# Kernel tuning notes

Measured on AMD Instinct MI355X. Metric: run time of the kernel, lower is better.

## Reference

```python
import jax, jax.numpy as jnp
import numpy as np

N_NODES = 100000
N_EDGES = 3200000
IN_F, HID_F, OUT_F = 512, 64, 16


def setup_inputs() -> dict:
    key = jax.random.key(0)
    k1, k2, k3, k4 = jax.random.split(key, 4)
    x = jax.random.normal(k1, (N_NODES, IN_F), dtype=jnp.float32)
    edge_index = jax.random.randint(k2, (2, N_EDGES), 0, N_NODES, dtype=jnp.int64)
    W1 = jax.random.normal(k3, (IN_F, HID_F), dtype=jnp.float32) * (1.0 / np.sqrt(IN_F))
    b1 = jnp.zeros((HID_F,), dtype=jnp.float32)
    W2 = jax.random.normal(k4, (HID_F, OUT_F), dtype=jnp.float32) * (1.0 / np.sqrt(HID_F))
    b2 = jnp.zeros((OUT_F,), dtype=jnp.float32)
    return {"x": x, "edge_index": edge_index, "W1": W1, "b1": b1, "W2": W2, "b2": b2}


def _gcn_norm(edge_index, n_nodes):
    # add self-loops (GCNConv default), edge_weight = 1
    loop = jnp.arange(n_nodes, dtype=edge_index.dtype)
    src = jnp.concatenate([edge_index[0], loop])
    dst = jnp.concatenate([edge_index[1], loop])
    ones = jnp.ones(src.shape[0], dtype=jnp.float32)
    deg = jax.ops.segment_sum(ones, dst, num_segments=n_nodes)
    dinv = jnp.where(deg > 0, jax.lax.rsqrt(deg), 0.0)
    norm = dinv[src] * dinv[dst]  # symmetric normalization D^-1/2 A D^-1/2
    return src, dst, norm


def _gcn_conv(h, src, dst, norm, W, b, n_nodes):
    h = h @ W                                 # project first (small GEMM)
    msg = h[src] * norm[:, None]              # gather + scale  [E+N, F_out]
    agg = jax.ops.segment_sum(msg, dst, num_segments=n_nodes)  # scatter-add
    return agg + b


def reference(x, edge_index, W1, b1, W2, b2):
    n = x.shape[0]
    src, dst, norm = _gcn_norm(edge_index, n)
    h = jax.nn.relu(_gcn_conv(x, src, dst, norm, W1, b1, n))
    # F.dropout with training=False is identity (eval-mode reference)
    h = _gcn_conv(h, src, dst, norm, W2, b2, n)
    return jax.nn.log_softmax(h, axis=1)
```

## Files before the change

### kernel.cpp

```cpp
#include <hip/hip_runtime.h>

#define NN    100000
#define NE    3200000
#define INF_  512
#define HIDF  64
#define OUTF  16
#define BR    128
#define NBUCK ((NN + BR - 1) / BR)
#define NGRP  8
#define SLICE 704
#define BSLOT (NGRP * SLICE)
#define NCUR  (NBUCK * NGRP)
#define NSLOT 72
#define EBLK  16384
#define NFB   ((NE + EBLK - 1) / EBLK)

typedef __bf16 bf16x8 __attribute__((ext_vector_type(8)));
typedef float  f32x4  __attribute__((ext_vector_type(4)));

__device__ inline unsigned short f2bfu(float f) {
    unsigned u = __builtin_bit_cast(unsigned, f);
    u += 0x7FFFu + ((u >> 16) & 1u);
    return (unsigned short)(u >> 16);
}
__device__ inline __bf16 bfbits(unsigned short h) {
    return __builtin_bit_cast(__bf16, h);
}
__device__ inline float bf2f(unsigned short h) {
    unsigned u = (unsigned)h << 16;
    return __builtin_bit_cast(float, u);
}

__global__ __launch_bounds__(256) void k_binit(int* __restrict__ bcur) {
    int i = blockIdx.x * 256 + threadIdx.x;
    if (i < NCUR) bcur[i] = (i >> 3) * BSLOT + (i & 7) * SLICE;
}

__global__ __launch_bounds__(256) void k_wconv(const float* __restrict__ W1,
                                               unsigned short* __restrict__ w1c) {
    int i = blockIdx.x * 256 + threadIdx.x;
    if (i < INF_ * HIDF) {
        int k = i >> 6, n = i & 63;
        w1c[((k >> 2) * 64 + n) * 4 + (k & 3)] = f2bfu(W1[i]);
    }
}

__global__ __launch_bounds__(256) void k_fillA(const int* __restrict__ src,
                                               const int* __restrict__ dst,
                                               int* __restrict__ bcur,
                                               unsigned int* __restrict__ pairs) {
    __shared__ int hist[NBUCK];
    __shared__ int rbase[NBUCK];
    int t = threadIdx.x;
    int e0 = blockIdx.x * EBLK;
    int e1 = (e0 + EBLK < NE) ? e0 + EBLK : NE;
    int grp = (int)(((long long)blockIdx.x * NGRP) / NFB);

    for (int b = t; b < NBUCK; b += 256) hist[b] = 0;
    __syncthreads();
    for (int e = e0 + t; e < e1; e += 256)
        atomicAdd(&hist[dst[e] >> 7], 1);
    __syncthreads();
    for (int b = t; b < NBUCK; b += 256) {
        int c = hist[b];
        rbase[b] = c ? atomicAdd(&bcur[b * NGRP + grp], c) : 0;
        hist[b] = 0;
    }
    __syncthreads();
    for (int e = e0 + t; e < e1; e += 256) {
        int s = src[e], d = dst[e];
        int b = d >> 7;
        int slot = atomicAdd(&hist[b], 1);
        pairs[rbase[b] + slot] = ((unsigned)s << 7) | (unsigned)(d & 127);
    }
}

__global__ __launch_bounds__(256) void k_fillB(const int* __restrict__ bcur,
                                               const unsigned int* __restrict__ pairs,
                                               int* __restrict__ re,
                                               float* __restrict__ dinv,
                                               int* __restrict__ csr) {
    __shared__ int cur_s[BR];
    int b  = blockIdx.x;
    int t  = threadIdx.x;
    int n0 = b * BR;
    int ncount = ((n0 + BR < NN) ? BR : NN - n0);

    if (t < BR) cur_s[t] = (n0 + t) * NSLOT;
    __syncthreads();

    for (int g = 0; g < NGRP; ++g) {
        int s0 = b * BSLOT + g * SLICE;
        int s1 = bcur[b * NGRP + g];
        for (int j = s0 + t; j < s1; j += 256) {
            unsigned int p = pairs[j];
            int pos = atomicAdd(&cur_s[p & 127u], 1);
            csr[pos] = (int)(p >> 7);
        }
    }
    __syncthreads();

    if (t < ncount) {
        int endp = cur_s[t];
        int n = n0 + t;
        re[n]   = endp;
        dinv[n] = rsqrtf((float)(endp - n * NSLOT + 1));
    }
}

#define GM 64

__global__ __launch_bounds__(256) void k_gemm1(const float* __restrict__ x,
                                               const unsigned short* __restrict__ w1c,
                                               const float* __restrict__ dinv,
                                               unsigned short* __restrict__ h1s) {
    __shared__ unsigned short bs[8192];
    int t    = threadIdx.x;
    int lane = t & 63;
    int w    = t >> 6;
    int m    = lane & 15;
    int kg   = lane >> 4;
    int mb   = blockIdx.x * GM;

    int rowi = mb + w * 16 + m;
    size_t xrow = (size_t)((rowi < NN) ? rowi : NN - 1);
    const float* xp = x + xrow * INF_ + kg * 4;

    f32x4 acc0 = {0.f,0.f,0.f,0.f}, acc1 = acc0, acc2 = acc0, acc3 = acc0;

    const uint4* w1c4 = (const uint4*)w1c;
    uint4* bs4 = (uint4*)bs;

    for (int kc = 0; kc < 4; ++kc) {
#pragma unroll
        for (int i = 0; i < 4; ++i)
            bs4[t + i * 256] = w1c4[kc * 1024 + t + i * 256];
        __syncthreads();

#pragma unroll
        for (int ks = 0; ks < 4; ++ks) {
            int ksg = kc * 4 + ks;
            float4 xa = *(const float4*)(xp + ksg * 32);
            float4 xb = *(const float4*)(xp + ksg * 32 + 16);
            bf16x8 A;
            A[0] = bfbits(f2bfu(xa.x)); A[1] = bfbits(f2bfu(xa.y));
            A[2] = bfbits(f2bfu(xa.z)); A[3] = bfbits(f2bfu(xa.w));
            A[4] = bfbits(f2bfu(xb.x)); A[5] = bfbits(f2bfu(xb.y));
            A[6] = bfbits(f2bfu(xb.z)); A[7] = bfbits(f2bfu(xb.w));

            int qq0 = ks * 8 + kg;
            int qq1 = qq0 + 4;
#pragma unroll
            for (int n0t = 0; n0t < 4; ++n0t) {
                ushort4 b0 = *(const ushort4*)&bs[(qq0 * 64 + n0t * 16 + m) * 4];
                ushort4 b1 = *(const ushort4*)&bs[(qq1 * 64 + n0t * 16 + m) * 4];
                bf16x8 B;
                B[0] = bfbits(b0.x); B[1] = bfbits(b0.y);
                B[2] = bfbits(b0.z); B[3] = bfbits(b0.w);
                B[4] = bfbits(b1.x); B[5] = bfbits(b1.y);
                B[6] = bfbits(b1.z); B[7] = bfbits(b1.w);
                f32x4 c = (n0t == 0) ? acc0 : (n0t == 1) ? acc1 : (n0t == 2) ? acc2 : acc3;
                c = __builtin_amdgcn_mfma_f32_16x16x32_bf16(A, B, c, 0, 0, 0);
                if      (n0t == 0) acc0 = c;
                else if (n0t == 1) acc1 = c;
                else if (n0t == 2) acc2 = c;
                else               acc3 = c;
            }
        }
        __syncthreads();
    }

#pragma unroll
    for (int r = 0; r < 4; ++r) {
        int node = mb + w * 16 + kg * 4 + r;
        if (node < NN) {
            float dv = dinv[node];
            size_t o = (size_t)node * HIDF + m;
            h1s[o +  0] = f2bfu(acc0[r] * dv);
            h1s[o + 16] = f2bfu(acc1[r] * dv);
            h1s[o + 32] = f2bfu(acc2[r] * dv);
            h1s[o + 48] = f2bfu(acc3[r] * dv);
        }
    }
}

__global__ __launch_bounds__(256) void k_hid2(const int* __restrict__ re,
                                              const int* __restrict__ csr,
                                              const float* __restrict__ dinv,
                                              const unsigned short* __restrict__ h1s,
                                              const float* __restrict__ b1,
                                              const float* __restrict__ W2,
                                              unsigned short* __restrict__ h2s) {
    __shared__ float w2s[HIDF * OUTF];
    __shared__ float b1s[HIDF];
    __shared__ float hbuf[4][HIDF];
    int t = threadIdx.x;
    for (int i = t; i < HIDF * OUTF; i += 256) w2s[i] = W2[i];
    if (t < HIDF) b1s[t] = b1[t];
    __syncthreads();

    int l = t & 63;
    int w = t >> 6;
    int g = l >> 4;
    int q = l & 15;
    int n = __builtin_amdgcn_readfirstlane(blockIdx.x * 4 + w);
    int row = n * NSLOT;
    int end = re[n];
    float dn = dinv[n];

    float a0 = 0.f, a1 = 0.f, a2 = 0.f, a3 = 0.f;

    int j = row;
    for (; j + 16 <= end; j += 16) {
        int4 scA = *(const int4*)&csr[j];
        int4 scB = *(const int4*)&csr[j + 4];
        int4 scC = *(const int4*)&csr[j + 8];
        int4 scD = *(const int4*)&csr[j + 12];
        int sA = (g & 2) ? ((g & 1) ? scA.w : scA.z) : ((g & 1) ? scA.y : scA.x);
        int sB = (g & 2) ? ((g & 1) ? scB.w : scB.z) : ((g & 1) ? scB.y : scB.x);
        int sC = (g & 2) ? ((g & 1) ? scC.w : scC.z) : ((g & 1) ? scC.y : scC.x);
        int sD = (g & 2) ? ((g & 1) ? scD.w : scD.z) : ((g & 1) ? scD.y : scD.x);
        ushort4 hA = *(const ushort4*)&h1s[(unsigned)(sA * HIDF + q * 4)];
        ushort4 hB = *(const ushort4*)&h1s[(unsigned)(sB * HIDF + q * 4)];
        ushort4 hC = *(const ushort4*)&h1s[(unsigned)(sC * HIDF + q * 4)];
        ushort4 hD = *(const ushort4*)&h1s[(unsigned)(sD * HIDF + q * 4)];
        a0 += (bf2f(hA.x) + bf2f(hB.x)) + (bf2f(hC.x) + bf2f(hD.x));
        a1 += (bf2f(hA.y) + bf2f(hB.y)) + (bf2f(hC.y) + bf2f(hD.y));
        a2 += (bf2f(hA.z) + bf2f(hB.z)) + (bf2f(hC.z) + bf2f(hD.z));
        a3 += (bf2f(hA.w) + bf2f(hB.w)) + (bf2f(hC.w) + bf2f(hD.w));
    }
    for (; j + 8 <= end; j += 8) {
        int4 scA = *(const int4*)&csr[j];
        int4 scB = *(const int4*)&csr[j + 4];
        int sA = (g & 2) ? ((g & 1) ? scA.w : scA.z) : ((g & 1) ? scA.y : scA.x);
        int sB = (g & 2) ? ((g & 1) ? scB.w : scB.z) : ((g & 1) ? scB.y : scB.x);
        ushort4 hA = *(const ushort4*)&h1s[(unsigned)(sA * HIDF + q * 4)];
        ushort4 hB = *(const ushort4*)&h1s[(unsigned)(sB * HIDF + q * 4)];
        a0 += bf2f(hA.x) + bf2f(hB.x);
        a1 += bf2f(hA.y) + bf2f(hB.y);
        a2 += bf2f(hA.z) + bf2f(hB.z);
        a3 += bf2f(hA.w) + bf2f(hB.w);
    }
    if (j + 4 <= end) {
        int4 sc = *(const int4*)&csr[j];
        int s = (g & 2) ? ((g & 1) ? sc.w : sc.z) : ((g & 1) ? sc.y : sc.x);
        ushort4 h = *(const ushort4*)&h1s[(unsigned)(s * HIDF + q * 4)];
        a0 += bf2f(h.x); a1 += bf2f(h.y); a2 += bf2f(h.z); a3 += bf2f(h.w);
        j += 4;
    }
    if (j + g < end) {
        int s = csr[j + g];
        ushort4 h = *(const ushort4*)&h1s[(unsigned)(s * HIDF + q * 4)];
        a0 += bf2f(h.x); a1 += bf2f(h.y); a2 += bf2f(h.z); a3 += bf2f(h.w);
    }

    a0 += __shfl_xor(a0, 16); a1 += __shfl_xor(a1, 16);
    a2 += __shfl_xor(a2, 16); a3 += __shfl_xor(a3, 16);
    a0 += __shfl_xor(a0, 32); a1 += __shfl_xor(a1, 32);
    a2 += __shfl_xor(a2, 32); a3 += __shfl_xor(a3, 32);

    ushort4 hs = *(const ushort4*)&h1s[(unsigned)(n * HIDF + q * 4)];
    a0 = fmaxf(fmaf(dn, a0 + bf2f(hs.x), b1s[q * 4 + 0]), 0.f);
    a1 = fmaxf(fmaf(dn, a1 + bf2f(hs.y), b1s[q * 4 + 1]), 0.f);
    a2 = fmaxf(fmaf(dn, a2 + bf2f(hs.z), b1s[q * 4 + 2]), 0.f);
    a3 = fmaxf(fmaf(dn, a3 + bf2f(hs.w), b1s[q * 4 + 3]), 0.f);
    if (g == 0) *(float4*)&hbuf[w][q * 4] = make_float4(a0, a1, a2, a3);
    __syncthreads();

    int o  = l & 15;
    int kg = l >> 4;
    const float* hb = hbuf[w];
    float s = 0.f;
#pragma unroll
    for (int i = 0; i < 16; ++i) {
        int k = kg * 16 + i;
        s = fmaf(hb[k], w2s[k * OUTF + o], s);
    }
    s += __shfl_xor(s, 16);
    s += __shfl_xor(s, 32);
    if (l < 16) h2s[(unsigned)(n * OUTF + o)] = f2bfu(dn * s);
}

__global__ __launch_bounds__(256) void k_out2(const int* __restrict__ re,
                                              const int* __restrict__ csr,
                                              const float* __restrict__ dinv,
                                              const unsigned short* __restrict__ h2s,
                                              const float* __restrict__ b2,
                                              float* __restrict__ out) {
    int t = blockIdx.x * 256 + threadIdx.x;
    int n = t >> 4;
    int f = t & 15;
    if (n >= NN) return;
    int row = n * NSLOT, end = re[n];
    float dn = dinv[n];
    float acc = bf2f(h2s[(unsigned)(n * OUTF + f)]);

    int j = row;
    for (; j + 8 <= end; j += 8) {
        int s0 = csr[j],     s1 = csr[j + 1], s2 = csr[j + 2], s3 = csr[j + 3];
        int s4 = csr[j + 4], s5 = csr[j + 5], s6 = csr[j + 6], s7 = csr[j + 7];
        float v0 = bf2f(h2s[(unsigned)(s0 * OUTF + f)]);
        float v1 = bf2f(h2s[(unsigned)(s1 * OUTF + f)]);
        float v2 = bf2f(h2s[(unsigned)(s2 * OUTF + f)]);
        float v3 = bf2f(h2s[(unsigned)(s3 * OUTF + f)]);
        float v4 = bf2f(h2s[(unsigned)(s4 * OUTF + f)]);
        float v5 = bf2f(h2s[(unsigned)(s5 * OUTF + f)]);
        float v6 = bf2f(h2s[(unsigned)(s6 * OUTF + f)]);
        float v7 = bf2f(h2s[(unsigned)(s7 * OUTF + f)]);
        acc += ((v0 + v1) + (v2 + v3)) + ((v4 + v5) + (v6 + v7));
    }
    for (; j + 4 <= end; j += 4) {
        int s0 = csr[j], s1 = csr[j + 1], s2 = csr[j + 2], s3 = csr[j + 3];
        float v0 = bf2f(h2s[(unsigned)(s0 * OUTF + f)]);
        float v1 = bf2f(h2s[(unsigned)(s1 * OUTF + f)]);
        float v2 = bf2f(h2s[(unsigned)(s2 * OUTF + f)]);
        float v3 = bf2f(h2s[(unsigned)(s3 * OUTF + f)]);
        acc += (v0 + v1) + (v2 + v3);
    }
    for (; j < end; ++j)
        acc += bf2f(h2s[(unsigned)(csr[j] * OUTF + f)]);

    float v = fmaf(dn, acc, b2[f]);

    float m = v;
#pragma unroll
    for (int mask = 1; mask < 16; mask <<= 1)
        m = fmaxf(m, __shfl_xor(m, mask, 16));
    float ex = __expf(v - m);
    float s  = ex;
#pragma unroll
    for (int mask = 1; mask < 16; mask <<= 1)
        s += __shfl_xor(s, mask, 16);
    out[(size_t)n * OUTF + f] = v - (m + __logf(s));
}

extern "C" void kernel_launch(void* const* d_in, const int* in_sizes, int n_in,
                              void* d_out, int out_size, void* d_ws, size_t ws_size,
                              hipStream_t stream) {
    const float* x  = (const float*)d_in[0];
    const int*   ei = (const int*)d_in[1];
    const float* W1 = (const float*)d_in[2];
    const float* b1 = (const float*)d_in[3];
    const float* W2 = (const float*)d_in[4];
    const float* b2 = (const float*)d_in[5];
    float*       out = (float*)d_out;

    char*  ws = (char*)d_ws;
    size_t o  = 0;
    auto alloc = [&](size_t bytes) {
        void* p = ws + o;
        o = (o + bytes + 1023) & ~(size_t)1023;
        return p;
    };
    int*            bcur  = (int*)           alloc((size_t)NCUR * 4);
    int*            re    = (int*)           alloc((size_t)NN * 4);
    int*            csr   = (int*)           alloc((size_t)NN * NSLOT * 4);
    unsigned int*   pairs = (unsigned int*)  alloc((size_t)NBUCK * BSLOT * 4);
    float*          dinv  = (float*)         alloc((size_t)NN * 4);
    unsigned short* w1c   = (unsigned short*)alloc((size_t)INF_ * HIDF * 2);
    unsigned short* h1s   = (unsigned short*)alloc((size_t)NN * HIDF * 2);
    unsigned short* h2s   = (unsigned short*)alloc((size_t)NN * OUTF * 2);
    if (o > ws_size) return;

    const int* esrc = ei;
    const int* edst = ei + NE;

    k_binit <<<(NCUR + 255) / 256, 256, 0, stream>>>(bcur);
    k_wconv <<<(INF_ * HIDF + 255) / 256, 256, 0, stream>>>(W1, w1c);
    k_fillA <<<NFB, 256, 0, stream>>>(esrc, edst, bcur, pairs);
    k_fillB <<<NBUCK, 256, 0, stream>>>(bcur, pairs, re, dinv, csr);

    k_gemm1 <<<(NN + GM - 1) / GM, 256, 0, stream>>>(x, w1c, dinv, h1s);
    k_hid2  <<<NN / 4, 256, 0, stream>>>(re, csr, dinv, h1s, b1, W2, h2s);
    k_out2  <<<(NN * OUTF + 255) / 256, 256, 0, stream>>>(re, csr, dinv, h2s, b2, out);
}
```

Baseline: 259.6 us.

## Overlap edge bucketing with GEMM in one launch and defer dinv scaling

Merges the edge-bucketing pass (fillA) and the dense x@W1 GEMM into a single kernel whose block ranges do different work, so the memory-bound bucketing and the GEMM run concurrently. The GEMM no longer depends on dinv, so the dinv scaling of h1 moves into fillB, which rereads and rewrites h1 in bf16 after computing degrees. The weight-conversion and cursor-init kernels are also merged into one launch. The cost is an extra read-modify-write pass over h1 and a second bf16 rounding step.

```diff
diff --git a/kernel.cpp b/kernel.cpp
--- a/kernel.cpp
+++ b/kernel.cpp
@@ -14,6 +14,8 @@
 #define NSLOT 72
 #define EBLK  16384
 #define NFB   ((NE + EBLK - 1) / EBLK)
+#define GM    64
+#define NGB   ((NN + GM - 1) / GM)
 
 typedef __bf16 bf16x8 __attribute__((ext_vector_type(8)));
 typedef float  f32x4  __attribute__((ext_vector_type(4)));
@@ -31,96 +33,63 @@
     return __builtin_bit_cast(float, u);
 }
 
-__global__ __launch_bounds__(256) void k_binit(int* __restrict__ bcur) {
-    int i = blockIdx.x * 256 + threadIdx.x;
-    if (i < NCUR) bcur[i] = (i >> 3) * BSLOT + (i & 7) * SLICE;
-}
-
-__global__ __launch_bounds__(256) void k_wconv(const float* __restrict__ W1,
-                                               unsigned short* __restrict__ w1c) {
-    int i = blockIdx.x * 256 + threadIdx.x;
-    if (i < INF_ * HIDF) {
+__global__ __launch_bounds__(256) void k_prep(const float* __restrict__ W1,
+                                              unsigned short* __restrict__ w1c,
+                                              int* __restrict__ bcur) {
+    int b = blockIdx.x, t = threadIdx.x;
+    if (b < 128) {
+        int i = b * 256 + t;
         int k = i >> 6, n = i & 63;
         w1c[((k >> 2) * 64 + n) * 4 + (k & 3)] = f2bfu(W1[i]);
-    }
-}
-
-__global__ __launch_bounds__(256) void k_fillA(const int* __restrict__ src,
-                                               const int* __restrict__ dst,
-                                               int* __restrict__ bcur,
-                                               unsigned int* __restrict__ pairs) {
-    __shared__ int hist[NBUCK];
-    __shared__ int rbase[NBUCK];
+    } else {
+        int i = (b - 128) * 256 + t;
+        if (i < NCUR) bcur[i] = (i >> 3) * BSLOT + (i & 7) * SLICE;
+    }
+}
+
+__global__ __launch_bounds__(256) void k_main(const float* __restrict__ x,
+                                              const unsigned short* __restrict__ w1c,
+                                              const int* __restrict__ src,
+                                              const int* __restrict__ dst,
+                                              int* __restrict__ bcur,
+                                              unsigned int* __restrict__ pairs,
+                                              unsigned short* __restrict__ h1s) {
+    __shared__ __align__(16) char smem[16384];
     int t = threadIdx.x;
-    int e0 = blockIdx.x * EBLK;
-    int e1 = (e0 + EBLK < NE) ? e0 + EBLK : NE;
-    int grp = (int)(((long long)blockIdx.x * NGRP) / NFB);
-
-    for (int b = t; b < NBUCK; b += 256) hist[b] = 0;
-    __syncthreads();
-    for (int e = e0 + t; e < e1; e += 256)
-        atomicAdd(&hist[dst[e] >> 7], 1);
-    __syncthreads();
-    for (int b = t; b < NBUCK; b += 256) {
-        int c = hist[b];
-        rbase[b] = c ? atomicAdd(&bcur[b * NGRP + grp], c) : 0;
-        hist[b] = 0;
-    }
-    __syncthreads();
-    for (int e = e0 + t; e < e1; e += 256) {
-        int s = src[e], d = dst[e];
-        int b = d >> 7;
-        int slot = atomicAdd(&hist[b], 1);
-        pairs[rbase[b] + slot] = ((unsigned)s << 7) | (unsigned)(d & 127);
-    }
-}
-
-__global__ __launch_bounds__(256) void k_fillB(const int* __restrict__ bcur,
-                                               const unsigned int* __restrict__ pairs,
-                                               int* __restrict__ re,
-                                               float* __restrict__ dinv,
-                                               int* __restrict__ csr) {
-    __shared__ int cur_s[BR];
-    int b  = blockIdx.x;
-    int t  = threadIdx.x;
-    int n0 = b * BR;
-    int ncount = ((n0 + BR < NN) ? BR : NN - n0);
-
-    if (t < BR) cur_s[t] = (n0 + t) * NSLOT;
-    __syncthreads();
-
-    for (int g = 0; g < NGRP; ++g) {
-        int s0 = b * BSLOT + g * SLICE;
-        int s1 = bcur[b * NGRP + g];
-        for (int j = s0 + t; j < s1; j += 256) {
-            unsigned int p = pairs[j];
-            int pos = atomicAdd(&cur_s[p & 127u], 1);
-            csr[pos] = (int)(p >> 7);
-        }
-    }
-    __syncthreads();
-
-    if (t < ncount) {
-        int endp = cur_s[t];
-        int n = n0 + t;
-        re[n]   = endp;
-        dinv[n] = rsqrtf((float)(endp - n * NSLOT + 1));
-    }
-}
-
-#define GM 64
-
-__global__ __launch_bounds__(256) void k_gemm1(const float* __restrict__ x,
-                                               const unsigned short* __restrict__ w1c,
-                                               const float* __restrict__ dinv,
-                                               unsigned short* __restrict__ h1s) {
-    __shared__ unsigned short bs[8192];
-    int t    = threadIdx.x;
+
+    if (blockIdx.x < NFB) {
+        int* hist  = (int*)smem;
+        int* rbase = ((int*)smem) + NBUCK;
+        int e0 = blockIdx.x * EBLK;
+        int e1 = (e0 + EBLK < NE) ? e0 + EBLK : NE;
+        int grp = (int)(((long long)blockIdx.x * NGRP) / NFB);
+
+        for (int b = t; b < NBUCK; b += 256) hist[b] = 0;
+        __syncthreads();
+        for (int e = e0 + t; e < e1; e += 256)
+            atomicAdd(&hist[dst[e] >> 7], 1);
+        __syncthreads();
+        for (int b = t; b < NBUCK; b += 256) {
+            int c = hist[b];
+            rbase[b] = c ? atomicAdd(&bcur[b * NGRP + grp], c) : 0;
+            hist[b] = 0;
+        }
+        __syncthreads();
+        for (int e = e0 + t; e < e1; e += 256) {
+            int s = src[e], d = dst[e];
+            int b = d >> 7;
+            int slot = atomicAdd(&hist[b], 1);
+            pairs[rbase[b] + slot] = ((unsigned)s << 7) | (unsigned)(d & 127);
+        }
+        return;
+    }
+
+    unsigned short* bs = (unsigned short*)smem;
     int lane = t & 63;
     int w    = t >> 6;
     int m    = lane & 15;
     int kg   = lane >> 4;
-    int mb   = blockIdx.x * GM;
+    int mb   = (blockIdx.x - NFB) * GM;
 
     int rowi = mb + w * 16 + m;
     size_t xrow = (size_t)((rowi < NN) ? rowi : NN - 1);
@@ -174,13 +143,55 @@
     for (int r = 0; r < 4; ++r) {
         int node = mb + w * 16 + kg * 4 + r;
         if (node < NN) {
-            float dv = dinv[node];
             size_t o = (size_t)node * HIDF + m;
-            h1s[o +  0] = f2bfu(acc0[r] * dv);
-            h1s[o + 16] = f2bfu(acc1[r] * dv);
-            h1s[o + 32] = f2bfu(acc2[r] * dv);
-            h1s[o + 48] = f2bfu(acc3[r] * dv);
-        }
+            h1s[o +  0] = f2bfu(acc0[r]);
+            h1s[o + 16] = f2bfu(acc1[r]);
+            h1s[o + 32] = f2bfu(acc2[r]);
+            h1s[o + 48] = f2bfu(acc3[r]);
+        }
+    }
+}
+
+__global__ __launch_bounds__(256) void k_fillB(const int* __restrict__ bcur,
+                                               const unsigned int* __restrict__ pairs,
+                                               int* __restrict__ re,
+                                               float* __restrict__ dinv,
+                                               int* __restrict__ csr,
+                                               unsigned short* __restrict__ h1s) {
+    __shared__ int   cur_s[BR];
+    __shared__ float dinv_s[BR];
+    int b  = blockIdx.x;
+    int t  = threadIdx.x;
+    int n0 = b * BR;
+    int ncount = ((n0 + BR < NN) ? BR : NN - n0);
+
+    if (t < BR) cur_s[t] = (n0 + t) * NSLOT;
+    __syncthreads();
+
+    for (int g = 0; g < NGRP; ++g) {
+        int s0 = b * BSLOT + g * SLICE;
+        int s1 = bcur[b * NGRP + g];
+        for (int j = s0 + t; j < s1; j += 256) {
+            unsigned int p = pairs[j];
+            int pos = atomicAdd(&cur_s[p & 127u], 1);
+            csr[pos] = (int)(p >> 7);
+        }
+    }
+    __syncthreads();
+
+    if (t < ncount) {
+        int endp = cur_s[t];
+        int n = n0 + t;
+        float dv = rsqrtf((float)(endp - n * NSLOT + 1));
+        re[n]    = endp;
+        dinv[n]  = dv;
+        dinv_s[t] = dv;
+    }
+    __syncthreads();
+
+    for (int i = t; i < ncount * HIDF; i += 256) {
+        unsigned idx = (unsigned)(n0 * HIDF + i);
+        h1s[idx] = f2bfu(bf2f(h1s[idx]) * dinv_s[i >> 6]);
     }
 }
 
@@ -365,12 +376,9 @@
     const int* esrc = ei;
     const int* edst = ei + NE;
 
-    k_binit <<<(NCUR + 255) / 256, 256, 0, stream>>>(bcur);
-    k_wconv <<<(INF_ * HIDF + 255) / 256, 256, 0, stream>>>(W1, w1c);
-    k_fillA <<<NFB, 256, 0, stream>>>(esrc, edst, bcur, pairs);
-    k_fillB <<<NBUCK, 256, 0, stream>>>(bcur, pairs, re, dinv, csr);
-
-    k_gemm1 <<<(NN + GM - 1) / GM, 256, 0, stream>>>(x, w1c, dinv, h1s);
+    k_prep  <<<128 + (NCUR + 255) / 256, 256, 0, stream>>>(W1, w1c, bcur);
+    k_main  <<<NFB + NGB, 256, 0, stream>>>(x, w1c, esrc, edst, bcur, pairs, h1s);
+    k_fillB <<<NBUCK, 256, 0, stream>>>(bcur, pairs, re, dinv, csr, h1s);
     k_hid2  <<<NN / 4, 256, 0, stream>>>(re, csr, dinv, h1s, b1, W2, h2s);
     k_out2  <<<(NN * OUTF + 255) / 256, 256, 0, stream>>>(re, csr, dinv, h2s, b2, out);
 }
```

New measurement: 247.2 us. 1.05x faster.
